# Kernel optimization log

Hardware: AMD Instinct MI355X
Metric: run time of the kernel (lower is better)

Reference implementation:

```python
import jax, jax.numpy as jnp
import numpy as np

N_NODES, N_EDGES, N_GRAPHS = 30000, 70000, 1024
TOWERS, F_IN, F_OUT, N_LAYERS = 5, 75, 15, 4
DEG_HIST = np.array([0.0, 100.0, 400.0, 300.0, 50.0], dtype=np.float32)
AVG_DEG_LOG = float((np.log(np.arange(len(DEG_HIST)) + 1.0) * DEG_HIST).sum() / DEG_HIST.sum())


def setup_inputs():
    key = jax.random.key(0)
    ks = jax.random.split(key, 16)
    g = lambda k, shp, fan: jax.random.normal(k, shp, jnp.float32) * (1.0 / np.sqrt(fan))
    return dict(
        x=jax.random.randint(ks[0], (N_NODES,), 0, 21),
        edge_index=jax.random.randint(ks[1], (2, N_EDGES), 0, N_NODES),
        edge_attr=jax.random.randint(ks[2], (N_EDGES,), 0, 4),
        batch=jnp.sort(jax.random.randint(ks[3], (N_NODES,), 0, N_GRAPHS)),
        node_emb=g(ks[4], (21, 75), 75),
        edge_emb=g(ks[5], (4, 50), 50),
        enc_w=g(ks[6], (N_LAYERS, 50, 75), 50),
        enc_b=jnp.zeros((N_LAYERS, 75), jnp.float32),
        pre_w=g(ks[7], (N_LAYERS, TOWERS, 3 * F_IN, F_IN), 3 * F_IN),
        pre_b=jnp.zeros((N_LAYERS, TOWERS, F_IN), jnp.float32),
        post_w=g(ks[8], (N_LAYERS, TOWERS, 13 * F_IN, F_OUT), 13 * F_IN),
        post_b=jnp.zeros((N_LAYERS, TOWERS, F_OUT), jnp.float32),
        lin_w=g(ks[9], (N_LAYERS, 75, 75), 75),
        lin_b=jnp.zeros((N_LAYERS, 75), jnp.float32),
        bn_g=jnp.ones((N_LAYERS, 75), jnp.float32),
        bn_b=jnp.zeros((N_LAYERS, 75), jnp.float32),
        mlp_w1=g(ks[10], (75, 50), 75), mlp_b1=jnp.zeros((50,), jnp.float32),
        mlp_w2=g(ks[11], (50, 25), 50), mlp_b2=jnp.zeros((25,), jnp.float32),
        mlp_w3=g(ks[12], (25, 1), 25), mlp_b3=jnp.zeros((1,), jnp.float32),
    )


def _pna_layer(h, src, dst, e_enc, pw, pb, qw, qb, lw, lb):
    n = h.shape[0]
    # message: cat[x_i, x_j, edge_enc] shared across towers, per-tower pre-NN
    msg = jnp.concatenate([h[dst], h[src], e_enc], axis=-1)            # [E, 3*F_in]
    m = jnp.einsum('ef,tfo->eto', msg, pw) + pb                        # [E, T, F_in]
    deg = jax.ops.segment_sum(jnp.ones((m.shape[0],), m.dtype), dst, n)
    has = (deg > 0)[:, None, None]
    cnt = jnp.maximum(deg, 1.0)[:, None, None]                         # clamp(1)
    mean = jax.ops.segment_sum(m, dst, n) / cnt
    mean_sq = jax.ops.segment_sum(m * m, dst, n) / cnt
    std = jnp.sqrt(jax.nn.relu(mean_sq - mean * mean) + 1e-5)
    mn = jnp.where(has, jax.ops.segment_min(m, dst, n), 0.0)
    mx = jnp.where(has, jax.ops.segment_max(m, dst, n), 0.0)
    agg = jnp.concatenate([mean, mn, mx, std], axis=-1)                # [N, T, 4*F_in]
    amp = jnp.log(cnt + 1.0) / AVG_DEG_LOG                             # amplification scaler
    scaled = jnp.concatenate([agg, agg * amp, agg / amp], axis=-1)     # [N, T, 12*F_in]
    post_in = jnp.concatenate(
        [jnp.broadcast_to(h[:, None, :], (n, TOWERS, F_IN)), scaled], axis=-1)  # [N, T, 13*F_in]
    out = jnp.einsum('ntf,tfo->nto', post_in, qw) + qb                 # [N, T, F_out]
    return out.reshape(n, TOWERS * F_OUT) @ lw + lb                    # [N, 75]


def _bn_relu(h, g, b):
    mu = h.mean(axis=0)
    var = h.var(axis=0)
    return jax.nn.relu((h - mu) * jax.lax.rsqrt(var + 1e-5) * g + b)


def reference(x, edge_index, edge_attr, batch, node_emb, edge_emb, enc_w, enc_b,
              pre_w, pre_b, post_w, post_b, lin_w, lin_b, bn_g, bn_b,
              mlp_w1, mlp_b1, mlp_w2, mlp_b2, mlp_w3, mlp_b3):
    h = node_emb[x]                      # [N, 75]
    e = edge_emb[edge_attr]              # [E, 50]
    src, dst = edge_index[0], edge_index[1]
    for l in range(N_LAYERS):
        e_enc = e @ enc_w[l] + enc_b[l]  # [E, 75]
        h = _bn_relu(_pna_layer(h, src, dst, e_enc, pre_w[l], pre_b[l],
                                post_w[l], post_b[l], lin_w[l], lin_b[l]),
                     bn_g[l], bn_b[l])
    hg = jax.ops.segment_sum(h, batch, N_GRAPHS)   # global_add_pool -> [G, 75]
    z = jax.nn.relu(hg @ mlp_w1 + mlp_b1)
    z = jax.nn.relu(z @ mlp_w2 + mlp_b2)
    return z @ mlp_w3 + mlp_b3
```

## Files before the change

### kernel.cpp

```cpp
#include <hip/hip_runtime.h>
#include <hip/hip_bf16.h>
#include <float.h>
#include <math.h>

#define NN 30000
#define NE 70000
#define NG 1024
#define NT 5
#define FI 75
#define NL 4

#define AMP_DENOM 1.1824939264481302f

#define ABW 832
#define AGW 1600
#define HBW 96
#define ZW 76

typedef __attribute__((ext_vector_type(8))) short bf16x8;
typedef __attribute__((ext_vector_type(4))) float f32x4;

__device__ __forceinline__ float bf2f(unsigned short u) {
    return __uint_as_float(((unsigned int)u) << 16);
}
__device__ __forceinline__ unsigned short f2bf(float f) {
    __hip_bfloat16 h = __float2bfloat16(f);
    return *reinterpret_cast<unsigned short*>(&h);
}

__global__ __launch_bounds__(256) void k_deg(const int* __restrict__ dst, int* __restrict__ deg) {
    int e = blockIdx.x * 256 + threadIdx.x;
    if (e < NE) atomicAdd(&deg[dst[e]], 1);
}

__global__ __launch_bounds__(1024) void k_scan(const int* __restrict__ deg, int* __restrict__ rowptr) {
    __shared__ int wsum[16];
    __shared__ int s_carry;
    int tid = threadIdx.x;
    int lane = tid & 63, wv = tid >> 6;
    if (tid == 0) s_carry = 0;
    __syncthreads();
    for (int base = 0; base < NN; base += 1024) {
        int i = base + tid;
        int v = (i < NN) ? deg[i] : 0;
        int x = v;
        #pragma unroll
        for (int off = 1; off < 64; off <<= 1) {
            int t = __shfl_up(x, off);
            if (lane >= off) x += t;
        }
        if (lane == 63) wsum[wv] = x;
        __syncthreads();
        if (tid < 16) {
            int y = wsum[tid];
            #pragma unroll
            for (int off = 1; off < 16; off <<= 1) {
                int t = __shfl_up(y, off);
                if (tid >= off) y += t;
            }
            wsum[tid] = y;
        }
        __syncthreads();
        int wbase = ((wv > 0) ? wsum[wv - 1] : 0) + s_carry;
        if (i < NN) rowptr[i] = wbase + x - v;
        int tot = wsum[15];
        __syncthreads();
        if (tid == 0) s_carry += tot;
    }
    __syncthreads();
    if (tid == 0) rowptr[NN] = s_carry;
}

__global__ __launch_bounds__(256) void k_scatter(const int* __restrict__ src, const int* __restrict__ dst,
                                                 const int* __restrict__ attr, const int* __restrict__ rowptr,
                                                 int* __restrict__ fill, int* __restrict__ csr) {
    int e = blockIdx.x * 256 + threadIdx.x;
    if (e < NE) {
        int d = dst[e];
        int pos = rowptr[d] + atomicAdd(&fill[d], 1);
        csr[pos] = src[e] | (attr[e] << 20);
    }
}

__global__ __launch_bounds__(256) void k_amp(const int* __restrict__ rowptr,
                                             float* __restrict__ amp, float* __restrict__ inv) {
    int n = blockIdx.x * 256 + threadIdx.x;
    if (n < NN) {
        int dg = rowptr[n + 1] - rowptr[n];
        float cnt = fmaxf((float)dg, 1.0f);
        float a = logf(cnt + 1.0f) * (1.0f / AMP_DENOM);
        amp[n] = a;
        inv[n] = 1.0f / a;
    }
}

__global__ __launch_bounds__(256) void k_h0(const int* __restrict__ x, const float* __restrict__ emb,
                                            unsigned short* __restrict__ hb) {
    int idx = blockIdx.x * 256 + threadIdx.x;
    if (idx < NN * HBW) {
        int n = idx / HBW, f = idx % HBW;
        hb[idx] = (f < FI) ? f2bf(emb[x[n] * FI + f]) : (unsigned short)0;
    }
}

__global__ __launch_bounds__(256) void k_wprep5(const float* __restrict__ post_w,
                                                unsigned short* __restrict__ Wp5) {
    int idx = blockIdx.x * 256 + threadIdx.x;
    if (idx >= NL * NT * 3 * 10 * 512) return;
    int e = idx & 7;
    int lane = (idx >> 3) & 63;
    int ks = (idx >> 9) % 10;
    int s = (idx / 5120) % 3;
    int t = (idx / 15360) % NT;
    int l = idx / 76800;
    int lr = lane & 15, lq = lane >> 4;
    int kk = ks * 32 + lq * 8 + e;
    float val = 0.0f;
    if (kk < 304 && lr < 15) {
        int stat = kk / 76, of = kk - stat * 76;
        if (of < 75)
            val = post_w[((size_t)(l * NT + t) * 975 + 75 + s * 300 + stat * 75 + of) * 15 + lr];
    }
    Wp5[idx] = f2bf(val);
}

__global__ __launch_bounds__(256) void k_wprep2f(const float* __restrict__ pre_w,
                                                 const float* __restrict__ post_w,
                                                 unsigned short* __restrict__ Wp2f) {
    int idx = blockIdx.x * 256 + threadIdx.x;
    if (idx >= NL * 52 * 3 * 512) return;
    int e = idx & 7;
    int lane = (idx >> 3) & 63;
    int ks = (idx >> 9) % 3;
    int nt = (idx / 1536) % 52;
    int l = idx / (1536 * 52);
    int lr = lane & 15, lq = lane >> 4;
    int j = nt * 16 + lr;
    int k = ks * 32 + lq * 8 + e;
    float val = 0.0f;
    if (k < 75 && j < 825) {
        if (j < 375) {
            int t = j / 75, o = j % 75;
            val = pre_w[((size_t)(l * NT + t) * 225 + k) * FI + o];
        } else if (j < 750) {
            int jm = j - 375;
            int t = jm / 75, o = jm % 75;
            val = pre_w[((size_t)(l * NT + t) * 225 + 75 + k) * FI + o];
        } else {
            int c = j - 750;
            int t = c / 15, o = c % 15;
            val = post_w[((size_t)(l * NT + t) * 975 + k) * 15 + o];
        }
    }
    Wp2f[idx] = f2bf(val);
}

__global__ __launch_bounds__(256) void k_wprep4(const float* __restrict__ lin_w,
                                                unsigned short* __restrict__ linTp) {
    int idx = blockIdx.x * 256 + threadIdx.x;
    if (idx >= NL * 5 * 3 * 512) return;
    int e = idx & 7;
    int lane = (idx >> 3) & 63;
    int ks = (idx >> 9) % 3;
    int nt = (idx / 1536) % 5;
    int l = idx / 7680;
    int lr = lane & 15, lq = lane >> 4;
    int c = nt * 16 + lr;
    int k = ks * 32 + lq * 8 + e;
    float v = 0.0f;
    if (k < 75 && c < 75) v = lin_w[(size_t)l * 5625 + k * 75 + c];
    linTp[idx] = f2bf(v);
}

__global__ __launch_bounds__(384) void k_tbl4(const float* __restrict__ edge_emb, const float* __restrict__ enc_w,
                                              const float* __restrict__ enc_b, const float* __restrict__ pre_w,
                                              const float* __restrict__ pre_b, float* __restrict__ tbl4) {
    __shared__ float e4[4][FI];
    int l = blockIdx.x;
    int tid = threadIdx.x;
    float* tbl = tbl4 + l * 1500;
    if (tid < 300) {
        int a = tid / FI, f = tid % FI;
        float acc = enc_b[l * FI + f];
        for (int k = 0; k < 50; k++)
            acc += edge_emb[a * 50 + k] * enc_w[(l * 50 + k) * FI + f];
        e4[a][f] = acc;
    }
    __syncthreads();
    for (int idx = tid; idx < 4 * 375; idx += 384) {
        int a = idx / 375, c = idx % 375;
        int t = c / FI, o = c % FI;
        const float* wp = pre_w + ((size_t)(l * NT + t) * 225 + 150) * FI + o;
        float acc = pre_b[(l * NT + t) * FI + o];
        for (int f = 0; f < FI; f++)
            acc += e4[a][f] * wp[f * FI];
        tbl[idx] = acc;
    }
}

__global__ __launch_bounds__(256) void k_bnh(const float* __restrict__ z, const float* __restrict__ bnsum,
                                             const float* __restrict__ bng, const float* __restrict__ bnb,
                                             unsigned short* __restrict__ hb) {
    __shared__ float s_sc[76], s_sh[76];
    int tid = threadIdx.x;
    if (tid < 76) {
        if (tid < 75) {
            float mu = bnsum[tid] * (1.0f / NN);
            float msq = bnsum[76 + tid] * (1.0f / NN);
            float var = msq - mu * mu;
            float sc = rsqrtf(var + 1e-5f) * bng[tid];
            s_sc[tid] = sc;
            s_sh[tid] = bnb[tid] - mu * sc;
        } else {
            s_sc[tid] = 0.0f;
            s_sh[tid] = 0.0f;
        }
    }
    __syncthreads();
    int idx = blockIdx.x * 256 + tid;
    if (idx < NN * 12) {
        int n = idx / 12, q = idx % 12;
        int c0 = q * 8;
        unsigned short r[8];
        if (c0 < 72) {
            float4 a = *(const float4*)&z[(size_t)n * ZW + c0];
            float4 b = *(const float4*)&z[(size_t)n * ZW + c0 + 4];
            float vv[8] = {a.x, a.y, a.z, a.w, b.x, b.y, b.z, b.w};
            #pragma unroll
            for (int j = 0; j < 8; j++)
                r[j] = f2bf(fmaxf(vv[j] * s_sc[c0 + j] + s_sh[c0 + j], 0.0f));
        } else if (c0 == 72) {
            float4 a = *(const float4*)&z[(size_t)n * ZW + 72];
            float vv[4] = {a.x, a.y, a.z, a.w};
            #pragma unroll
            for (int j = 0; j < 8; j++)
                r[j] = (j < 3) ? f2bf(fmaxf(vv[j] * s_sc[72 + j] + s_sh[72 + j], 0.0f))
                               : (unsigned short)0;
        } else {
            #pragma unroll
            for (int j = 0; j < 8; j++) r[j] = 0;
        }
        *(uint4*)&hb[(size_t)n * HBW + c0] = *(uint4*)r;
    }
}

__global__ __launch_bounds__(256) void k_preab(const unsigned short* __restrict__ hb,
                                               const unsigned short* __restrict__ Wp2f,
                                               int l, __hip_bfloat16* __restrict__ ABH) {
    __shared__ __align__(16) unsigned short sA[128 * 104];
    int tid = threadIdx.x;
    int m0 = blockIdx.x * 128;
    int jt0 = blockIdx.y * 13;

    const uint4* hsrc = (const uint4*)hb;
    for (int c = tid; c < 128 * 12; c += 256) {
        int r = c / 12, q = c % 12;
        int n = m0 + r;
        uint4 v = make_uint4(0, 0, 0, 0);
        if (n < NN) v = hsrc[(size_t)n * 12 + q];
        *(uint4*)&sA[r * 104 + q * 8] = v;
    }
    __syncthreads();

    int w = tid >> 6, lane = tid & 63;
    int mw = w * 32;
    int lr = lane & 15, lq = lane >> 4;

    bf16x8 af[2][3];
    #pragma unroll
    for (int mt = 0; mt < 2; mt++)
        #pragma unroll
        for (int ks = 0; ks < 3; ks++)
            af[mt][ks] = *(const bf16x8*)&sA[(mw + mt * 16 + lr) * 104 + ks * 32 + lq * 8];

    f32x4 acc[13][2];
    #pragma unroll
    for (int nt = 0; nt < 13; nt++)
        #pragma unroll
        for (int mt = 0; mt < 2; mt++)
            acc[nt][mt] = (f32x4){0.0f, 0.0f, 0.0f, 0.0f};

    const unsigned short* wp = Wp2f + ((size_t)l * 52 + jt0) * 3 * 512;
    #pragma unroll
    for (int nt = 0; nt < 13; nt++) {
        #pragma unroll
        for (int ks = 0; ks < 3; ks++) {
            bf16x8 bf = *(const bf16x8*)&wp[(nt * 3 + ks) * 512 + lane * 8];
            acc[nt][0] = __builtin_amdgcn_mfma_f32_16x16x32_bf16(bf, af[0][ks], acc[nt][0], 0, 0, 0);
            acc[nt][1] = __builtin_amdgcn_mfma_f32_16x16x32_bf16(bf, af[1][ks], acc[nt][1], 0, 0, 0);
        }
    }

    unsigned short* abo = (unsigned short*)ABH;
    int j0 = jt0 * 16;
    #pragma unroll
    for (int mt = 0; mt < 2; mt++) {
        int n = m0 + mw + mt * 16 + lr;
        if (n < NN) {
            #pragma unroll
            for (int nt = 0; nt < 13; nt++) {
                int c0 = j0 + nt * 16 + lq * 4;
                ushort4 us;
                us.x = f2bf(acc[nt][mt][0]);
                us.y = f2bf(acc[nt][mt][1]);
                us.z = f2bf(acc[nt][mt][2]);
                us.w = f2bf(acc[nt][mt][3]);
                *(ushort4*)&abo[(size_t)n * ABW + c0] = us;
            }
        }
    }
}

__global__ __launch_bounds__(256, 1) void k_gather(const __hip_bfloat16* __restrict__ ABH,
                                                   const float* __restrict__ tbl,
                                                   const int* __restrict__ rowptr, const int* __restrict__ csr,
                                                   unsigned short* __restrict__ AGG) {
    __shared__ float s_tbl[1500];
    int tid = threadIdx.x;
    for (int i = tid; i < 1500; i += 256) s_tbl[i] = tbl[i];
    __syncthreads();

    int w = tid >> 6, l = tid & 63;
    int n = blockIdx.x * 4 + w;
    int base = rowptr[n];
    int dg = rowptr[n + 1] - base;

    float sum[6], ss[6], mn[6], mx[6];
    #pragma unroll
    for (int j = 0; j < 6; j++) { sum[j] = 0.f; ss[j] = 0.f; mn[j] = FLT_MAX; mx[j] = -FLT_MAX; }

    const unsigned short* abu = (const unsigned short*)ABH;
    int k = 0;
    for (; k + 3 < dg; k += 4) {
        int pk0 = csr[base + k], pk1 = csr[base + k + 1];
        int pk2 = csr[base + k + 2], pk3 = csr[base + k + 3];
        const unsigned short* bp0 = abu + (size_t)(pk0 & 0xFFFFF) * ABW + 375;
        const unsigned short* bp1 = abu + (size_t)(pk1 & 0xFFFFF) * ABW + 375;
        const unsigned short* bp2 = abu + (size_t)(pk2 & 0xFFFFF) * ABW + 375;
        const unsigned short* bp3 = abu + (size_t)(pk3 & 0xFFFFF) * ABW + 375;
        const float* tp0 = s_tbl + (pk0 >> 20) * 375;
        const float* tp1 = s_tbl + (pk1 >> 20) * 375;
        const float* tp2 = s_tbl + (pk2 >> 20) * 375;
        const float* tp3 = s_tbl + (pk3 >> 20) * 375;
        #pragma unroll
        for (int j = 0; j < 6; j++) {
            int f = l + 64 * j;
            if (f < 375) {
                float v0 = bf2f(bp0[f]) + tp0[f];
                float v1 = bf2f(bp1[f]) + tp1[f];
                float v2 = bf2f(bp2[f]) + tp2[f];
                float v3 = bf2f(bp3[f]) + tp3[f];
                sum[j] += (v0 + v1) + (v2 + v3);
                ss[j] += (v0 * v0 + v1 * v1) + (v2 * v2 + v3 * v3);
                mn[j] = fminf(mn[j], fminf(fminf(v0, v1), fminf(v2, v3)));
                mx[j] = fmaxf(mx[j], fmaxf(fmaxf(v0, v1), fmaxf(v2, v3)));
            }
        }
    }
    for (; k < dg; k++) {
        int pk0 = csr[base + k];
        const unsigned short* bp0 = abu + (size_t)(pk0 & 0xFFFFF) * ABW + 375;
        const float* tp0 = s_tbl + (pk0 >> 20) * 375;
        #pragma unroll
        for (int j = 0; j < 6; j++) {
            int f = l + 64 * j;
            if (f < 375) {
                float v0 = bf2f(bp0[f]) + tp0[f];
                sum[j] += v0; ss[j] += v0 * v0;
                mn[j] = fminf(mn[j], v0); mx[j] = fmaxf(mx[j], v0);
            }
        }
    }

    unsigned short* out = AGG + (size_t)n * AGW;
    if (dg > 0) {
        float rc = 1.0f / (float)dg;
        const unsigned short* ap = abu + (size_t)n * ABW;
        #pragma unroll
        for (int j = 0; j < 6; j++) {
            int f = l + 64 * j;
            if (f < 375) {
                int t = f / 75, of = f - t * 75;
                int o = t * 320 + of;
                float Af = bf2f(ap[f]);
                float mean = sum[j] * rc;
                float var = ss[j] * rc - mean * mean;
                out[o]       = f2bf(Af + mean);
                out[o + 76]  = f2bf(Af + mn[j]);
                out[o + 152] = f2bf(Af + mx[j]);
                out[o + 228] = f2bf(sqrtf(fmaxf(var, 0.0f) + 1e-5f));
            }
        }
    } else {
        unsigned short zz = 0;
        unsigned short sd = f2bf(0.0031622776601683794f);
        #pragma unroll
        for (int j = 0; j < 6; j++) {
            int f = l + 64 * j;
            if (f < 375) {
                int t = f / 75, of = f - t * 75;
                int o = t * 320 + of;
                out[o] = zz; out[o + 76] = zz; out[o + 152] = zz; out[o + 228] = sd;
            }
        }
    }
    for (int i = l; i < 80; i += 64) out[(i >> 4) * 320 + 304 + (i & 15)] = 0;
    if (l < 20) out[(l >> 2) * 320 + (l & 3) * 76 + 75] = 0;
}

#define LOAD_A(buf, t)                                                        \
    {                                                                         \
        _Pragma("unroll")                                                     \
        for (int ks = 0; ks < 10; ks++)                                       \
            buf[ks] = *(const bf16x8*)&ap[(t) * 320 + ks * 32 + lq * 8];      \
    }

#define DO_TOWER(t, buf)                                                               \
    {                                                                                  \
        const unsigned short* wp = Wp5 + (size_t)(l * NT + (t)) * 3 * 10 * 512;        \
        f32x4 ac0 = {0, 0, 0, 0}, ac1 = {0, 0, 0, 0}, ac2 = {0, 0, 0, 0};              \
        _Pragma("unroll")                                                              \
        for (int ks = 0; ks < 10; ks++) {                                              \
            bf16x8 b0 = *(const bf16x8*)&wp[(0 * 10 + ks) * 512 + lane * 8];           \
            bf16x8 b1 = *(const bf16x8*)&wp[(1 * 10 + ks) * 512 + lane * 8];           \
            bf16x8 b2 = *(const bf16x8*)&wp[(2 * 10 + ks) * 512 + lane * 8];           \
            ac0 = __builtin_amdgcn_mfma_f32_16x16x32_bf16(b0, buf[ks], ac0, 0, 0, 0);  \
            ac1 = __builtin_amdgcn_mfma_f32_16x16x32_bf16(b1, buf[ks], ac1, 0, 0, 0);  \
            ac2 = __builtin_amdgcn_mfma_f32_16x16x32_bf16(b2, buf[ks], ac2, 0, 0, 0);  \
        }                                                                              \
        _Pragma("unroll")                                                              \
        for (int r = 0; r < 4; r++) {                                                  \
            int f = lq * 4 + r;                                                        \
            if (f < 15) {                                                              \
                float qb = post_b[(l * NT + (t)) * 15 + f];                            \
                float y = ac0[r] + amp * ac1[r] + inv * ac2[r] + htv[t][r] + qb;       \
                s_y[(w * 16 + lr) * 104 + (t) * 15 + f] = f2bf(y);                     \
            }                                                                          \
        }                                                                              \
    }

__global__ __launch_bounds__(256, 1) void k_post(const __hip_bfloat16* __restrict__ ABH,
                                                 const unsigned short* __restrict__ AGG,
                                                 const unsigned short* __restrict__ Wp5,
                                                 const unsigned short* __restrict__ linTp,
                                                 const float* __restrict__ amp_a, const float* __restrict__ inv_a,
                                                 const float* __restrict__ post_b, const float* __restrict__ lin_b,
                                                 int l, float* __restrict__ z, float* __restrict__ bnsum) {
    __shared__ __align__(16) unsigned short s_y[64 * 104];
    __shared__ float s_bn[152];

    int tid = threadIdx.x;
    int n0 = blockIdx.x * 64;
    int w = tid >> 6, lane = tid & 63;
    int lr = lane & 15, lq = lane >> 4;

    if (tid < 152) s_bn[tid] = 0.0f;
    for (int i = tid; i < 64 * 29; i += 256) {
        int r = i / 29, c = 75 + i % 29;
        s_y[r * 104 + c] = 0;
    }

    const unsigned short* abu = (const unsigned short*)ABH;
    int mynode = n0 + w * 16 + lr;
    bool nv = (mynode < NN);
    int mclamp = nv ? mynode : (NN - 1);
    float amp = amp_a[mclamp], inv = inv_a[mclamp];
    const unsigned short* ap = AGG + (size_t)mclamp * AGW;

    bf16x8 aA[10], aB[10];
    LOAD_A(aA, 0)
    float htv[5][4];
    #pragma unroll
    for (int t = 0; t < 5; t++) {
        #pragma unroll
        for (int r = 0; r < 4; r++) {
            int f = lq * 4 + r;
            int fc = (f < 15) ? f : 14;
            htv[t][r] = bf2f(abu[(size_t)mclamp * ABW + 750 + t * 15 + fc]);
        }
    }

    LOAD_A(aB, 1)
    DO_TOWER(0, aA)
    LOAD_A(aA, 2)
    DO_TOWER(1, aB)
    LOAD_A(aB, 3)
    DO_TOWER(2, aA)
    LOAD_A(aA, 4)
    DO_TOWER(3, aB)
    DO_TOWER(4, aA)
    __syncthreads();

    const unsigned short* lp = linTp + (size_t)l * 5 * 3 * 512;
    bf16x8 ya[3];
    #pragma unroll
    for (int ks = 0; ks < 3; ks++)
        ya[ks] = *(const bf16x8*)&s_y[(w * 16 + lr) * 104 + ks * 32 + lq * 8];

    #pragma unroll
    for (int nt = 0; nt < 5; nt++) {
        f32x4 a2 = {0, 0, 0, 0};
        #pragma unroll
        for (int ks = 0; ks < 3; ks++) {
            bf16x8 bb = *(const bf16x8*)&lp[(nt * 3 + ks) * 512 + lane * 8];
            a2 = __builtin_amdgcn_mfma_f32_16x16x32_bf16(bb, ya[ks], a2, 0, 0, 0);
        }
        int c0 = nt * 16 + lq * 4;
        float v[4], vm[4], vm2[4];
        #pragma unroll
        for (int r = 0; r < 4; r++) {
            int c = c0 + r;
            v[r] = (c < 75) ? (a2[r] + lin_b[l * 75 + c]) : 0.0f;
            bool ok = (c < 75) && nv;
            vm[r] = ok ? v[r] : 0.0f;
            vm2[r] = ok ? v[r] * v[r] : 0.0f;
        }
        if (nv) {
            if (c0 + 3 < 75) {
                float4 st = make_float4(v[0], v[1], v[2], v[3]);
                *(float4*)&z[(size_t)mynode * ZW + c0] = st;
            } else {
                #pragma unroll
                for (int r = 0; r < 4; r++)
                    if (c0 + r < 75) z[(size_t)mynode * ZW + c0 + r] = v[r];
            }
        }
        #pragma unroll
        for (int r = 0; r < 4; r++) {
            #pragma unroll
            for (int off = 1; off < 16; off <<= 1) {
                vm[r] += __shfl_xor(vm[r], off);
                vm2[r] += __shfl_xor(vm2[r], off);
            }
        }
        if (lr == 0) {
            #pragma unroll
            for (int r = 0; r < 4; r++) {
                int c = c0 + r;
                if (c < 75) {
                    atomicAdd(&s_bn[c], vm[r]);
                    atomicAdd(&s_bn[76 + c], vm2[r]);
                }
            }
        }
    }
    __syncthreads();
    if (tid < 75) {
        atomicAdd(&bnsum[tid], s_bn[tid]);
        atomicAdd(&bnsum[76 + tid], s_bn[76 + tid]);
    }
}

__global__ __launch_bounds__(256) void k_pool(const float* __restrict__ z, const float* __restrict__ bnsum3,
                                              const float* __restrict__ bng, const float* __restrict__ bnb,
                                              const int* __restrict__ batch, float* __restrict__ hg) {
    __shared__ float s_sc[75], s_sh[75];
    int tid = threadIdx.x;
    if (tid < 75) {
        float mu = bnsum3[tid] * (1.0f / NN);
        float msq = bnsum3[76 + tid] * (1.0f / NN);
        float var = msq - mu * mu;
        float sc = rsqrtf(var + 1e-5f) * bng[tid];
        s_sc[tid] = sc;
        s_sh[tid] = bnb[tid] - mu * sc;
    }
    __syncthreads();
    int idx = blockIdx.x * 256 + tid;
    if (idx < NN * 75) {
        int n = idx / 75, f = idx % 75;
        float v = fmaxf(z[(size_t)n * ZW + f] * s_sc[f] + s_sh[f], 0.0f);
        atomicAdd(&hg[batch[n] * 75 + f], v);
    }
}

__global__ __launch_bounds__(64) void k_mlp(const float* __restrict__ hg,
                                            const float* __restrict__ w1, const float* __restrict__ b1,
                                            const float* __restrict__ w2, const float* __restrict__ b2,
                                            const float* __restrict__ w3, const float* __restrict__ b3,
                                            float* __restrict__ out) {
    __shared__ float zin[75], z1[50], z2[25];
    int g = blockIdx.x, tid = threadIdx.x;
    for (int k = tid; k < 75; k += 64) zin[k] = hg[g * 75 + k];
    __syncthreads();
    if (tid < 50) {
        float acc = b1[tid];
        for (int k = 0; k < 75; k++) acc += zin[k] * w1[k * 50 + tid];
        z1[tid] = fmaxf(acc, 0.0f);
    }
    __syncthreads();
    if (tid < 25) {
        float acc = b2[tid];
        for (int k = 0; k < 50; k++) acc += z1[k] * w2[k * 25 + tid];
        z2[tid] = fmaxf(acc, 0.0f);
    }
    __syncthreads();
    if (tid == 0) {
        float acc = b3[0];
        for (int k = 0; k < 25; k++) acc += z2[k] * w3[k];
        out[g] = acc;
    }
}

extern "C" void kernel_launch(void* const* d_in, const int* in_sizes, int n_in,
                              void* d_out, int out_size, void* d_ws, size_t ws_size,
                              hipStream_t stream) {
    const int* x        = (const int*)d_in[0];
    const int* ei       = (const int*)d_in[1];
    const int* eattr    = (const int*)d_in[2];
    const int* batch    = (const int*)d_in[3];
    const float* node_emb = (const float*)d_in[4];
    const float* edge_emb = (const float*)d_in[5];
    const float* enc_w  = (const float*)d_in[6];
    const float* enc_b  = (const float*)d_in[7];
    const float* pre_w  = (const float*)d_in[8];
    const float* pre_b  = (const float*)d_in[9];
    const float* post_w = (const float*)d_in[10];
    const float* post_b = (const float*)d_in[11];
    const float* lin_w  = (const float*)d_in[12];
    const float* lin_b  = (const float*)d_in[13];
    const float* bn_g   = (const float*)d_in[14];
    const float* bn_b   = (const float*)d_in[15];
    const float* w1     = (const float*)d_in[16];
    const float* b1     = (const float*)d_in[17];
    const float* w2     = (const float*)d_in[18];
    const float* b2     = (const float*)d_in[19];
    const float* w3     = (const float*)d_in[20];
    const float* b3     = (const float*)d_in[21];

    char* p = (char*)d_ws;
    auto carve = [&](size_t bytes) -> char* {
        char* r = p;
        p += ((bytes + 255) & ~(size_t)255);
        return r;
    };
    __hip_bfloat16* ABH = (__hip_bfloat16*)carve((size_t)NN * ABW * 2);
    unsigned short* AGG = (unsigned short*)carve((size_t)NN * AGW * 2);
    float* z     = (float*)carve((size_t)NN * ZW * 4);
    unsigned short* hb = (unsigned short*)carve((size_t)NN * HBW * 2);
    unsigned short* Wp2f  = (unsigned short*)carve((size_t)NL * 52 * 3 * 512 * 2);
    unsigned short* Wp5   = (unsigned short*)carve((size_t)NL * NT * 3 * 10 * 512 * 2);
    unsigned short* linTp = (unsigned short*)carve((size_t)NL * 5 * 3 * 512 * 2);
    float* tbl4  = (float*)carve((size_t)NL * 1500 * 4);
    int* deg     = (int*)carve(NN * 4);
    int* rowptr  = (int*)carve((NN + 1) * 4);
    int* fill    = (int*)carve(NN * 4);
    int* csr     = (int*)carve(NE * 4);
    float* bnsum = (float*)carve((size_t)NL * 152 * 4);
    float* amp_a = (float*)carve(NN * 4);
    float* inv_a = (float*)carve(NN * 4);
    float* hg    = (float*)carve((size_t)NG * 75 * 4);

    hipMemsetAsync(deg, 0, NN * 4, stream);
    hipMemsetAsync(fill, 0, NN * 4, stream);
    hipMemsetAsync(hg, 0, (size_t)NG * 75 * 4, stream);
    hipMemsetAsync(bnsum, 0, (size_t)NL * 152 * 4, stream);

    k_deg<<<(NE + 255) / 256, 256, 0, stream>>>(ei + NE, deg);
    k_scan<<<1, 1024, 0, stream>>>(deg, rowptr);
    k_scatter<<<(NE + 255) / 256, 256, 0, stream>>>(ei, ei + NE, eattr, rowptr, fill, csr);
    k_amp<<<(NN + 255) / 256, 256, 0, stream>>>(rowptr, amp_a, inv_a);
    k_h0<<<(NN * HBW + 255) / 256, 256, 0, stream>>>(x, node_emb, hb);
    k_wprep5<<<(NL * NT * 3 * 10 * 512 + 255) / 256, 256, 0, stream>>>(post_w, Wp5);
    k_wprep2f<<<(NL * 52 * 3 * 512 + 255) / 256, 256, 0, stream>>>(pre_w, post_w, Wp2f);
    k_wprep4<<<(NL * 5 * 3 * 512 + 255) / 256, 256, 0, stream>>>(lin_w, linTp);
    k_tbl4<<<NL, 384, 0, stream>>>(edge_emb, enc_w, enc_b, pre_w, pre_b, tbl4);

    for (int l = 0; l < NL; l++) {
        if (l > 0)
            k_bnh<<<(NN * 12 + 255) / 256, 256, 0, stream>>>(
                z, bnsum + (l - 1) * 152, bn_g + (l - 1) * 75, bn_b + (l - 1) * 75, hb);
        k_preab<<<dim3((NN + 127) / 128, 4), 256, 0, stream>>>(hb, Wp2f, l, ABH);
        k_gather<<<NN / 4, 256, 0, stream>>>(ABH, tbl4 + l * 1500, rowptr, csr, AGG);
        k_post<<<(NN + 63) / 64, 256, 0, stream>>>(ABH, AGG, Wp5, linTp, amp_a, inv_a,
                                                   post_b, lin_b, l, z, bnsum + l * 152);
    }

    k_pool<<<(NN * 75 + 255) / 256, 256, 0, stream>>>(z, bnsum + 3 * 152, bn_g + 3 * 75, bn_b + 3 * 75,
                                                      batch, hg);
    k_mlp<<<NG, 64, 0, stream>>>(hg, w1, b1, w2, b2, w3, b3, (float*)d_out);
}
```

Before: 612.2 us.

## Split post towers across wave pairs and relax launch bounds in gather/post

k_post now covers 32 nodes per block instead of 64. Each 16-node group is handled by two waves: one computes towers 0-2 and output tiles 0-2, the other computes towers 3-4 and tiles 3-4. This doubles the grid and cuts the serial MFMA chain per wave, which should help occupancy and latency hiding. k_gather drops the min-blocks hint from its launch bounds and unrolls by 2 instead of 4 to lower register pressure and raise occupancy, at the cost of fewer independent loads in flight. The tower split is uneven (3 vs 2), so the two waves carry unequal work.

```diff
diff --git a/kernel.cpp b/kernel.cpp
--- a/kernel.cpp
+++ b/kernel.cpp
@@ -311,10 +311,10 @@
     }
 }
 
-__global__ __launch_bounds__(256, 1) void k_gather(const __hip_bfloat16* __restrict__ ABH,
-                                                   const float* __restrict__ tbl,
-                                                   const int* __restrict__ rowptr, const int* __restrict__ csr,
-                                                   unsigned short* __restrict__ AGG) {
+__global__ __launch_bounds__(256) void k_gather(const __hip_bfloat16* __restrict__ ABH,
+                                                const float* __restrict__ tbl,
+                                                const int* __restrict__ rowptr, const int* __restrict__ csr,
+                                                unsigned short* __restrict__ AGG) {
     __shared__ float s_tbl[1500];
     int tid = threadIdx.x;
     for (int i = tid; i < 1500; i += 256) s_tbl[i] = tbl[i];
@@ -331,33 +331,26 @@
 
     const unsigned short* abu = (const unsigned short*)ABH;
     int k = 0;
-    for (; k + 3 < dg; k += 4) {
+    for (; k + 1 < dg; k += 2) {
         int pk0 = csr[base + k], pk1 = csr[base + k + 1];
-        int pk2 = csr[base + k + 2], pk3 = csr[base + k + 3];
         const unsigned short* bp0 = abu + (size_t)(pk0 & 0xFFFFF) * ABW + 375;
         const unsigned short* bp1 = abu + (size_t)(pk1 & 0xFFFFF) * ABW + 375;
-        const unsigned short* bp2 = abu + (size_t)(pk2 & 0xFFFFF) * ABW + 375;
-        const unsigned short* bp3 = abu + (size_t)(pk3 & 0xFFFFF) * ABW + 375;
         const float* tp0 = s_tbl + (pk0 >> 20) * 375;
         const float* tp1 = s_tbl + (pk1 >> 20) * 375;
-        const float* tp2 = s_tbl + (pk2 >> 20) * 375;
-        const float* tp3 = s_tbl + (pk3 >> 20) * 375;
         #pragma unroll
         for (int j = 0; j < 6; j++) {
             int f = l + 64 * j;
             if (f < 375) {
                 float v0 = bf2f(bp0[f]) + tp0[f];
                 float v1 = bf2f(bp1[f]) + tp1[f];
-                float v2 = bf2f(bp2[f]) + tp2[f];
-                float v3 = bf2f(bp3[f]) + tp3[f];
-                sum[j] += (v0 + v1) + (v2 + v3);
-                ss[j] += (v0 * v0 + v1 * v1) + (v2 * v2 + v3 * v3);
-                mn[j] = fminf(mn[j], fminf(fminf(v0, v1), fminf(v2, v3)));
-                mx[j] = fmaxf(mx[j], fmaxf(fmaxf(v0, v1), fmaxf(v2, v3)));
+                sum[j] += v0 + v1;
+                ss[j] += v0 * v0 + v1 * v1;
+                mn[j] = fminf(mn[j], fminf(v0, v1));
+                mx[j] = fmaxf(mx[j], fmaxf(v0, v1));
             }
         }
     }
-    for (; k < dg; k++) {
+    if (k < dg) {
         int pk0 = csr[base + k];
         const unsigned short* bp0 = abu + (size_t)(pk0 & 0xFFFFF) * ABW + 375;
         const float* tp0 = s_tbl + (pk0 >> 20) * 375;
@@ -434,115 +427,128 @@
             if (f < 15) {                                                              \
                 float qb = post_b[(l * NT + (t)) * 15 + f];                            \
                 float y = ac0[r] + amp * ac1[r] + inv * ac2[r] + htv[t][r] + qb;       \
-                s_y[(w * 16 + lr) * 104 + (t) * 15 + f] = f2bf(y);                     \
+                s_y[(u * 16 + lr) * 104 + (t) * 15 + f] = f2bf(y);                     \
             }                                                                          \
         }                                                                              \
     }
 
-__global__ __launch_bounds__(256, 1) void k_post(const __hip_bfloat16* __restrict__ ABH,
-                                                 const unsigned short* __restrict__ AGG,
-                                                 const unsigned short* __restrict__ Wp5,
-                                                 const unsigned short* __restrict__ linTp,
-                                                 const float* __restrict__ amp_a, const float* __restrict__ inv_a,
-                                                 const float* __restrict__ post_b, const float* __restrict__ lin_b,
-                                                 int l, float* __restrict__ z, float* __restrict__ bnsum) {
-    __shared__ __align__(16) unsigned short s_y[64 * 104];
+#define LOAD_HT(t)                                                                     \
+    {                                                                                  \
+        _Pragma("unroll")                                                              \
+        for (int r = 0; r < 4; r++) {                                                  \
+            int f = lq * 4 + r;                                                        \
+            int fc = (f < 15) ? f : 14;                                                \
+            htv[t][r] = bf2f(abu[(size_t)mclamp * ABW + 750 + (t) * 15 + fc]);         \
+        }                                                                              \
+    }
+
+#define DO_LIN(nt)                                                                     \
+    {                                                                                  \
+        f32x4 a2 = {0, 0, 0, 0};                                                       \
+        _Pragma("unroll")                                                              \
+        for (int ks = 0; ks < 3; ks++) {                                               \
+            bf16x8 bb = *(const bf16x8*)&lp[((nt) * 3 + ks) * 512 + lane * 8];         \
+            a2 = __builtin_amdgcn_mfma_f32_16x16x32_bf16(bb, ya[ks], a2, 0, 0, 0);     \
+        }                                                                              \
+        int c0 = (nt) * 16 + lq * 4;                                                   \
+        float v[4], vm[4], vm2[4];                                                     \
+        _Pragma("unroll")                                                              \
+        for (int r = 0; r < 4; r++) {                                                  \
+            int c = c0 + r;                                                            \
+            v[r] = (c < 75) ? (a2[r] + lin_b[l * 75 + c]) : 0.0f;                      \
+            bool ok = (c < 75) && nv;                                                  \
+            vm[r] = ok ? v[r] : 0.0f;                                                  \
+            vm2[r] = ok ? v[r] * v[r] : 0.0f;                                          \
+        }                                                                              \
+        if (nv) {                                                                      \
+            if (c0 + 3 < 75) {                                                         \
+                float4 st = make_float4(v[0], v[1], v[2], v[3]);                       \
+                *(float4*)&z[(size_t)mynode * ZW + c0] = st;                           \
+            } else {                                                                   \
+                _Pragma("unroll")                                                      \
+                for (int r = 0; r < 4; r++)                                            \
+                    if (c0 + r < 75) z[(size_t)mynode * ZW + c0 + r] = v[r];           \
+            }                                                                          \
+        }                                                                              \
+        _Pragma("unroll")                                                              \
+        for (int r = 0; r < 4; r++) {                                                  \
+            _Pragma("unroll")                                                          \
+            for (int off = 1; off < 16; off <<= 1) {                                   \
+                vm[r] += __shfl_xor(vm[r], off);                                       \
+                vm2[r] += __shfl_xor(vm2[r], off);                                     \
+            }                                                                          \
+        }                                                                              \
+        if (lr == 0) {                                                                 \
+            _Pragma("unroll")                                                          \
+            for (int r = 0; r < 4; r++) {                                              \
+                int c = c0 + r;                                                        \
+                if (c < 75) {                                                          \
+                    atomicAdd(&s_bn[c], vm[r]);                                        \
+                    atomicAdd(&s_bn[76 + c], vm2[r]);                                  \
+                }                                                                      \
+            }                                                                          \
+        }                                                                              \
+    }
+
+__global__ __launch_bounds__(256) void k_post(const __hip_bfloat16* __restrict__ ABH,
+                                              const unsigned short* __restrict__ AGG,
+                                              const unsigned short* __restrict__ Wp5,
+                                              const unsigned short* __restrict__ linTp,
+                                              const float* __restrict__ amp_a, const float* __restrict__ inv_a,
+                                              const float* __restrict__ post_b, const float* __restrict__ lin_b,
+                                              int l, float* __restrict__ z, float* __restrict__ bnsum) {
+    __shared__ __align__(16) unsigned short s_y[32 * 104];
     __shared__ float s_bn[152];
 
     int tid = threadIdx.x;
-    int n0 = blockIdx.x * 64;
+    int n0 = blockIdx.x * 32;
     int w = tid >> 6, lane = tid & 63;
+    int u = w >> 1, g = w & 1;
     int lr = lane & 15, lq = lane >> 4;
 
     if (tid < 152) s_bn[tid] = 0.0f;
-    for (int i = tid; i < 64 * 29; i += 256) {
+    for (int i = tid; i < 32 * 29; i += 256) {
         int r = i / 29, c = 75 + i % 29;
         s_y[r * 104 + c] = 0;
     }
 
     const unsigned short* abu = (const unsigned short*)ABH;
-    int mynode = n0 + w * 16 + lr;
+    int mynode = n0 + u * 16 + lr;
     bool nv = (mynode < NN);
     int mclamp = nv ? mynode : (NN - 1);
     float amp = amp_a[mclamp], inv = inv_a[mclamp];
     const unsigned short* ap = AGG + (size_t)mclamp * AGW;
 
     bf16x8 aA[10], aB[10];
-    LOAD_A(aA, 0)
     float htv[5][4];
-    #pragma unroll
-    for (int t = 0; t < 5; t++) {
-        #pragma unroll
-        for (int r = 0; r < 4; r++) {
-            int f = lq * 4 + r;
-            int fc = (f < 15) ? f : 14;
-            htv[t][r] = bf2f(abu[(size_t)mclamp * ABW + 750 + t * 15 + fc]);
-        }
-    }
-
-    LOAD_A(aB, 1)
-    DO_TOWER(0, aA)
-    LOAD_A(aA, 2)
-    DO_TOWER(1, aB)
-    LOAD_A(aB, 3)
-    DO_TOWER(2, aA)
-    LOAD_A(aA, 4)
-    DO_TOWER(3, aB)
-    DO_TOWER(4, aA)
+
+    if (g == 0) {
+        LOAD_A(aA, 0)
+        LOAD_HT(0) LOAD_HT(1) LOAD_HT(2)
+        LOAD_A(aB, 1)
+        DO_TOWER(0, aA)
+        LOAD_A(aA, 2)
+        DO_TOWER(1, aB)
+        DO_TOWER(2, aA)
+    } else {
+        LOAD_A(aA, 3)
+        LOAD_HT(3) LOAD_HT(4)
+        LOAD_A(aB, 4)
+        DO_TOWER(3, aA)
+        DO_TOWER(4, aB)
+    }
     __syncthreads();
 
     const unsigned short* lp = linTp + (size_t)l * 5 * 3 * 512;
     bf16x8 ya[3];
     #pragma unroll
     for (int ks = 0; ks < 3; ks++)
-        ya[ks] = *(const bf16x8*)&s_y[(w * 16 + lr) * 104 + ks * 32 + lq * 8];
-
-    #pragma unroll
-    for (int nt = 0; nt < 5; nt++) {
-        f32x4 a2 = {0, 0, 0, 0};
-        #pragma unroll
-        for (int ks = 0; ks < 3; ks++) {
-            bf16x8 bb = *(const bf16x8*)&lp[(nt * 3 + ks) * 512 + lane * 8];
-            a2 = __builtin_amdgcn_mfma_f32_16x16x32_bf16(bb, ya[ks], a2, 0, 0, 0);
-        }
-        int c0 = nt * 16 + lq * 4;
-        float v[4], vm[4], vm2[4];
-        #pragma unroll
-        for (int r = 0; r < 4; r++) {
-            int c = c0 + r;
-            v[r] = (c < 75) ? (a2[r] + lin_b[l * 75 + c]) : 0.0f;
-            bool ok = (c < 75) && nv;
-            vm[r] = ok ? v[r] : 0.0f;
-            vm2[r] = ok ? v[r] * v[r] : 0.0f;
-        }
-        if (nv) {
-            if (c0 + 3 < 75) {
-                float4 st = make_float4(v[0], v[1], v[2], v[3]);
-                *(float4*)&z[(size_t)mynode * ZW + c0] = st;
-            } else {
-                #pragma unroll
-                for (int r = 0; r < 4; r++)
-                    if (c0 + r < 75) z[(size_t)mynode * ZW + c0 + r] = v[r];
-            }
-        }
-        #pragma unroll
-        for (int r = 0; r < 4; r++) {
-            #pragma unroll
-            for (int off = 1; off < 16; off <<= 1) {
-                vm[r] += __shfl_xor(vm[r], off);
-                vm2[r] += __shfl_xor(vm2[r], off);
-            }
-        }
-        if (lr == 0) {
-            #pragma unroll
-            for (int r = 0; r < 4; r++) {
-                int c = c0 + r;
-                if (c < 75) {
-                    atomicAdd(&s_bn[c], vm[r]);
-                    atomicAdd(&s_bn[76 + c], vm2[r]);
-                }
-            }
-        }
+        ya[ks] = *(const bf16x8*)&s_y[(u * 16 + lr) * 104 + ks * 32 + lq * 8];
+
+    if (g == 0) {
+        DO_LIN(0) DO_LIN(1) DO_LIN(2)
+    } else {
+        DO_LIN(3) DO_LIN(4)
     }
     __syncthreads();
     if (tid < 75) {
@@ -671,7 +677,7 @@
                 z, bnsum + (l - 1) * 152, bn_g + (l - 1) * 75, bn_b + (l - 1) * 75, hb);
         k_preab<<<dim3((NN + 127) / 128, 4), 256, 0, stream>>>(hb, Wp2f, l, ABH);
         k_gather<<<NN / 4, 256, 0, stream>>>(ABH, tbl4 + l * 1500, rowptr, csr, AGG);
-        k_post<<<(NN + 63) / 64, 256, 0, stream>>>(ABH, AGG, Wp5, linTp, amp_a, inv_a,
+        k_post<<<(NN + 31) / 32, 256, 0, stream>>>(ABH, AGG, Wp5, linTp, amp_a, inv_a,
                                                    post_b, lin_b, l, z, bnsum + l * 152);
     }
 
```

Measured after the change: 623.5 us. About the same (+1.8%).
